# Optimization experiments

Hardware: AMD Instinct MI355X
Metric: run time of the kernel (lower is better)

## Reference

```python
import jax, jax.numpy as jnp
import numpy as np

N, H, O, E, K = 131072, 128, 128, 8, 2


def setup_inputs() -> dict:
    key = jax.random.key(0)
    k1, k2, k3, k4 = jax.random.split(key, 4)
    x = jax.random.normal(k1, (N, H), dtype=jnp.float32)
    w_gate = jax.random.normal(k2, (H, E), dtype=jnp.float32) * 0.02
    w_noise = jax.random.normal(k3, (H, E), dtype=jnp.float32) * 0.02
    w_expert = jax.random.normal(k4, (E, H, O), dtype=jnp.float32) * (1.0 / np.sqrt(H))
    b_expert = jnp.zeros((E, O), dtype=jnp.float32)
    return {"x": x, "w_gate": w_gate, "w_noise": w_noise,
            "w_expert": w_expert, "b_expert": b_expert, "top_k": K}


def _gates(x, w_gate, top_k):
    # Noisy top-k gating (eval mode: noise term w_noise is inactive).
    logits = x @ w_gate                              # [N, E]
    top_vals, top_idx = jax.lax.top_k(logits, top_k)  # [N, K]
    top_gates = jax.nn.softmax(top_vals, axis=-1)     # renormalize over top-k
    n = logits.shape[0]
    rows = jnp.arange(n)[:, None]                     # [N, 1]
    gates = jnp.zeros_like(logits).at[rows, top_idx].set(top_gates)  # [N, E] sparse
    return gates


def reference(x, w_gate, w_noise, w_expert, b_expert, top_k):
    gates = _gates(x, w_gate, top_k)                                  # [N, E]
    # Dense (mathematically identical) dispatch/combine: every expert FFN
    # applied per token, weighted by its (mostly-zero) gate.
    expert_out = jnp.einsum('nh,eho->neo', x, w_expert) + b_expert     # [N, E, O]
    out = jnp.einsum('ne,neo->no', gates, expert_out)                  # [N, O]
    return out
```

## Files before the change

kernel.cpp:

```cpp
#include <hip/hip_runtime.h>
#include <math.h>

typedef __bf16 bf16x8 __attribute__((ext_vector_type(8)));
typedef float f32x16 __attribute__((ext_vector_type(16)));

#define NTOK 131072
#define HDIM 128
#define ODIM 128
#define NEXP 8

__device__ __forceinline__ unsigned short f2bf(float f){
  union { float f; unsigned u; } v; v.f = f;
  unsigned r = v.u + 0x7FFFu + ((v.u >> 16) & 1u);
  return (unsigned short)(r >> 16);
}

__global__ void pack_w(const float* __restrict__ we, const float* __restrict__ be,
                       unsigned short* __restrict__ pw){
  int f = blockIdx.x * 256 + threadIdx.x;
  int l  = f & 63;
  int kt = (f >> 6) % 9;
  int emt = f / (64 * 9);
  int mt = emt & 3;
  int e  = emt >> 2;
  int o  = (mt << 5) + (l & 31);
  unsigned short vals[8];
#pragma unroll
  for (int j = 0; j < 8; ++j){
    int kl = ((l >> 5) << 3) + j;
    float v;
    if (kt < 8){
      int h = kt * 16 + kl;
      v = we[(e * HDIM + h) * ODIM + o];
    } else {
      v = (kl == 0) ? be[e * ODIM + o] : 0.0f;
    }
    vals[j] = f2bf(v);
  }
  *(bf16x8*)(pw + (size_t)f * 8) = *(bf16x8*)vals;
}

__launch_bounds__(256, 2)
__global__ void moe_fused(const float* __restrict__ x, const float* __restrict__ wg,
                          const unsigned short* __restrict__ pw, float* __restrict__ out){
  __shared__ char lds[33792 + 4096 + 2048];
  float* xs            = (float*)lds;
  unsigned short* frag = (unsigned short*)lds;
  float* tb            = (float*)lds;
  float* wgl           = (float*)(lds + 33792);
  float* glds          = (float*)(lds + 33792 + 4096);

  int t = threadIdx.x;
  size_t tokbase = (size_t)blockIdx.x * 64;

  ((float4*)wgl)[t] = ((const float4*)wg)[t];
  {
    const float4* xsrc = (const float4*)(x + tokbase * HDIM);
#pragma unroll
    for (int i = 0; i < 8; ++i){
      int idx = i * 256 + t;
      int tok = idx >> 5, c = idx & 31;
      *(float4*)&xs[tok * 132 + c * 4] = xsrc[idx];
    }
  }
  __syncthreads();

  float4 cv[8];
#pragma unroll
  for (int i = 0; i < 8; ++i)
    cv[i] = *(float4*)&xs[(t >> 2) * 132 + (t & 3) * 32 + i * 4];

  if (t < 64){
    float lg[8];
#pragma unroll
    for (int e = 0; e < 8; ++e) lg[e] = 0.0f;
#pragma unroll 8
    for (int c = 0; c < 32; ++c){
      float4 v = *(float4*)&xs[t * 132 + c * 4];
      const float* wr = wgl + c * 32;
#pragma unroll
      for (int e = 0; e < 8; ++e)
        lg[e] += v.x * wr[e] + v.y * wr[8 + e] + v.z * wr[16 + e] + v.w * wr[24 + e];
    }
    int i1 = 0; float v1 = lg[0];
#pragma unroll
    for (int e = 1; e < 8; ++e) if (lg[e] > v1){ v1 = lg[e]; i1 = e; }
    int i2 = -1; float v2 = -3.4e38f;
#pragma unroll
    for (int e = 0; e < 8; ++e) if (e != i1 && lg[e] > v2){ v2 = lg[e]; i2 = e; }
    float ex = __expf(v2 - v1);
    float inv = 1.0f / (1.0f + ex);
#pragma unroll
    for (int e = 0; e < 8; ++e)
      glds[e * 64 + t] = (e == i1) ? inv : ((e == i2) ? ex * inv : 0.0f);
  }
  __syncthreads();

  {
    int tokL = t >> 2, q = t & 3, tg = tokL >> 5;
#pragma unroll
    for (int jb = 0; jb < 4; ++jb){
      int h0 = q * 32 + jb * 8;
      int kt = h0 >> 4;
      int lslot = (tokL & 31) + 32 * ((h0 >> 3) & 1);
      float4 a = cv[2 * jb], b = cv[2 * jb + 1];
      unsigned long long lo = (unsigned long long)f2bf(a.x)
                            | ((unsigned long long)f2bf(a.y) << 16)
                            | ((unsigned long long)f2bf(a.z) << 32)
                            | ((unsigned long long)f2bf(a.w) << 48);
      unsigned long long hi = (unsigned long long)f2bf(b.x)
                            | ((unsigned long long)f2bf(b.y) << 16)
                            | ((unsigned long long)f2bf(b.z) << 32)
                            | ((unsigned long long)f2bf(b.w) << 48);
      unsigned long long* dst =
        (unsigned long long*)&frag[(((tg * 9) + kt) * 64 + lslot) * 8];
      dst[0] = lo; dst[1] = hi;
    }
    if (t < 128){
      int btg = t >> 6, bl = t & 63;
      unsigned long long* dst =
        (unsigned long long*)&frag[(((btg * 9) + 8) * 64 + bl) * 8];
      dst[0] = (bl < 32) ? 0x3F80ull : 0ull;
      dst[1] = 0ull;
    }
  }
  __syncthreads();

  int w = t >> 6, l = t & 63, l32 = l & 31, lh = l >> 5;

  bf16x8 xb0[9], xb1[9];
#pragma unroll
  for (int kt = 0; kt < 9; ++kt){
    xb0[kt] = *(const bf16x8*)&frag[((0 * 9 + kt) * 64 + l) * 8];
    xb1[kt] = *(const bf16x8*)&frag[((1 * 9 + kt) * 64 + l) * 8];
  }
  __syncthreads();

  f32x16 zero16;
#pragma unroll
  for (int i = 0; i < 16; ++i) zero16[i] = 0.0f;
  f32x16 tot0 = zero16, tot1 = zero16;

  const bf16x8* pwp = (const bf16x8*)pw;
#pragma unroll 1
  for (int e = 0; e < 8; ++e){
    float g0 = glds[e * 64 + l32];
    float g1 = glds[e * 64 + 32 + l32];
    const bf16x8* ap = pwp + ((size_t)(e * 4 + w) * 9) * 64 + l;
    f32x16 p0 = zero16, p1 = zero16;
#pragma unroll
    for (int kt = 0; kt < 9; ++kt){
      bf16x8 a = ap[kt * 64];
      p0 = __builtin_amdgcn_mfma_f32_32x32x16_bf16(a, xb0[kt], p0, 0, 0, 0);
      p1 = __builtin_amdgcn_mfma_f32_32x32x16_bf16(a, xb1[kt], p1, 0, 0, 0);
    }
#pragma unroll
    for (int r = 0; r < 16; ++r){
      tot0[r] += g0 * p0[r];
      tot1[r] += g1 * p1[r];
    }
  }

  {
#pragma unroll
    for (int rg = 0; rg < 4; ++rg){
      int o = w * 32 + rg * 8 + lh * 4;
      {
        int trow = 0 * 32 + l32;
        int cs = (o >> 2) ^ l32;
        *(float4*)&tb[trow * 128 + cs * 4] =
          make_float4(tot0[rg * 4 + 0], tot0[rg * 4 + 1], tot0[rg * 4 + 2], tot0[rg * 4 + 3]);
      }
      {
        int trow = 1 * 32 + l32;
        int cs = (o >> 2) ^ l32;
        *(float4*)&tb[trow * 128 + cs * 4] =
          make_float4(tot1[rg * 4 + 0], tot1[rg * 4 + 1], tot1[rg * 4 + 2], tot1[rg * 4 + 3]);
      }
    }
  }
  __syncthreads();
#pragma unroll
  for (int i = 0; i < 8; ++i){
    int idx = i * 256 + t;
    int trow = idx >> 5, c = idx & 31;
    int cs = c ^ (trow & 31);
    float4 v = *(float4*)&tb[trow * 128 + cs * 4];
    *(float4*)(out + (tokbase + trow) * ODIM + c * 4) = v;
  }
}

extern "C" void kernel_launch(void* const* d_in, const int* in_sizes, int n_in,
                              void* d_out, int out_size, void* d_ws, size_t ws_size,
                              hipStream_t stream){
  const float* x  = (const float*)d_in[0];
  const float* wg = (const float*)d_in[1];
  const float* we = (const float*)d_in[3];
  const float* be = (const float*)d_in[4];
  float* out = (float*)d_out;

  unsigned short* pw = (unsigned short*)d_ws;

  pack_w   <<<72,   256, 0, stream>>>(we, be, pw);
  moe_fused<<<2048, 256, 0, stream>>>(x, wg, pw, out);
}
```

Before: 161.3 us.

## Split MoE into gating/pack and LDS-staged weight GEMM kernels

Splits the fused kernel in two. One kernel computes the gates with a 4-way parallel logit reduction and writes bf16 MFMA-fragment x and transposed gates to workspace. A second GEMM kernel stages half of one output tile's expert weights in LDS and processes 512 tokens per block, reusing those weights across 16 token groups instead of reloading them from global memory per 64 tokens. The bias moves out of the MFMA k-loop into a scalar epilogue. The cost is an extra kernel launch plus a global round trip for the bf16 x fragments and the gates.

```diff
diff --git a/kernel.cpp b/kernel.cpp
--- a/kernel.cpp
+++ b/kernel.cpp
@@ -15,41 +15,27 @@
   return (unsigned short)(r >> 16);
 }
 
-__global__ void pack_w(const float* __restrict__ we, const float* __restrict__ be,
-                       unsigned short* __restrict__ pw){
+__global__ void pack_w(const float* __restrict__ we, unsigned short* __restrict__ pw){
   int f = blockIdx.x * 256 + threadIdx.x;
-  int l  = f & 63;
-  int kt = (f >> 6) % 9;
-  int emt = f / (64 * 9);
-  int mt = emt & 3;
-  int e  = emt >> 2;
-  int o  = (mt << 5) + (l & 31);
+  int l   = f & 63;
+  int kt2 = (f >> 6) & 3;
+  int e   = (f >> 8) & 7;
+  int h   = (f >> 11) & 1;
+  int ot  = (f >> 12) & 3;
+  int o = ot * 32 + (l & 31);
+  int kbase = (h * 4 + kt2) * 16 + ((l >> 5) << 3);
   unsigned short vals[8];
 #pragma unroll
-  for (int j = 0; j < 8; ++j){
-    int kl = ((l >> 5) << 3) + j;
-    float v;
-    if (kt < 8){
-      int h = kt * 16 + kl;
-      v = we[(e * HDIM + h) * ODIM + o];
-    } else {
-      v = (kl == 0) ? be[e * ODIM + o] : 0.0f;
-    }
-    vals[j] = f2bf(v);
-  }
+  for (int j = 0; j < 8; ++j)
+    vals[j] = f2bf(we[(e * HDIM + kbase + j) * ODIM + o]);
   *(bf16x8*)(pw + (size_t)f * 8) = *(bf16x8*)vals;
 }
 
-__launch_bounds__(256, 2)
-__global__ void moe_fused(const float* __restrict__ x, const float* __restrict__ wg,
-                          const unsigned short* __restrict__ pw, float* __restrict__ out){
-  __shared__ char lds[33792 + 4096 + 2048];
-  float* xs            = (float*)lds;
-  unsigned short* frag = (unsigned short*)lds;
-  float* tb            = (float*)lds;
-  float* wgl           = (float*)(lds + 33792);
-  float* glds          = (float*)(lds + 33792 + 4096);
-
+__global__ void gating_pack(const float* __restrict__ x, const float* __restrict__ wg,
+                            float* __restrict__ gates_t, unsigned short* __restrict__ xf){
+  __shared__ float xs[64 * 128];
+  __shared__ float wgl[128 * 8];
+  __shared__ float plg[64 * 36];
   int t = threadIdx.x;
   size_t tokbase = (size_t)blockIdx.x * 64;
 
@@ -60,28 +46,35 @@
     for (int i = 0; i < 8; ++i){
       int idx = i * 256 + t;
       int tok = idx >> 5, c = idx & 31;
-      *(float4*)&xs[tok * 132 + c * 4] = xsrc[idx];
+      *(float4*)&xs[tok * 128 + ((c ^ (tok & 7)) << 2)] = xsrc[idx];
     }
   }
   __syncthreads();
 
-  float4 cv[8];
-#pragma unroll
-  for (int i = 0; i < 8; ++i)
-    cv[i] = *(float4*)&xs[(t >> 2) * 132 + (t & 3) * 32 + i * 4];
+  {
+    int tok = t & 63, q = t >> 6;
+    float lg[8];
+#pragma unroll
+    for (int e = 0; e < 8; ++e) lg[e] = 0.0f;
+#pragma unroll
+    for (int i = 0; i < 8; ++i){
+      int c = q * 8 + i;
+      float4 v = *(float4*)&xs[tok * 128 + ((c ^ (tok & 7)) << 2)];
+      const float* wr = wgl + c * 32;
+#pragma unroll
+      for (int e = 0; e < 8; ++e)
+        lg[e] += v.x * wr[e] + v.y * wr[8 + e] + v.z * wr[16 + e] + v.w * wr[24 + e];
+    }
+    *(float4*)&plg[tok * 36 + q * 8]     = make_float4(lg[0], lg[1], lg[2], lg[3]);
+    *(float4*)&plg[tok * 36 + q * 8 + 4] = make_float4(lg[4], lg[5], lg[6], lg[7]);
+  }
+  __syncthreads();
 
   if (t < 64){
     float lg[8];
 #pragma unroll
-    for (int e = 0; e < 8; ++e) lg[e] = 0.0f;
-#pragma unroll 8
-    for (int c = 0; c < 32; ++c){
-      float4 v = *(float4*)&xs[t * 132 + c * 4];
-      const float* wr = wgl + c * 32;
-#pragma unroll
-      for (int e = 0; e < 8; ++e)
-        lg[e] += v.x * wr[e] + v.y * wr[8 + e] + v.z * wr[16 + e] + v.w * wr[24 + e];
-    }
+    for (int e = 0; e < 8; ++e)
+      lg[e] = plg[t * 36 + e] + plg[t * 36 + 8 + e] + plg[t * 36 + 16 + e] + plg[t * 36 + 24 + e];
     int i1 = 0; float v1 = lg[0];
 #pragma unroll
     for (int e = 1; e < 8; ++e) if (lg[e] > v1){ v1 = lg[e]; i1 = e; }
@@ -92,17 +85,21 @@
     float inv = 1.0f / (1.0f + ex);
 #pragma unroll
     for (int e = 0; e < 8; ++e)
-      glds[e * 64 + t] = (e == i1) ? inv : ((e == i2) ? ex * inv : 0.0f);
-  }
-  __syncthreads();
+      gates_t[(size_t)e * NTOK + tokbase + t] = (e == i1) ? inv : ((e == i2) ? ex * inv : 0.0f);
+  }
 
   {
-    int tokL = t >> 2, q = t & 3, tg = tokL >> 5;
+    int tokL = t >> 2, q = t & 3;
+    float4 cv[8];
+#pragma unroll
+    for (int i = 0; i < 8; ++i)
+      cv[i] = *(float4*)&xs[tokL * 128 + (((q * 8 + i) ^ (tokL & 7)) << 2)];
+    size_t tgG = (size_t)blockIdx.x * 2 + (tokL >> 5);
 #pragma unroll
     for (int jb = 0; jb < 4; ++jb){
       int h0 = q * 32 + jb * 8;
       int kt = h0 >> 4;
-      int lslot = (tokL & 31) + 32 * ((h0 >> 3) & 1);
+      int lslot = (tokL & 31) + 32 * (jb & 1);
       float4 a = cv[2 * jb], b = cv[2 * jb + 1];
       unsigned long long lo = (unsigned long long)f2bf(a.x)
                             | ((unsigned long long)f2bf(a.y) << 16)
@@ -112,82 +109,120 @@
                             | ((unsigned long long)f2bf(b.y) << 16)
                             | ((unsigned long long)f2bf(b.z) << 32)
                             | ((unsigned long long)f2bf(b.w) << 48);
-      unsigned long long* dst =
-        (unsigned long long*)&frag[(((tg * 9) + kt) * 64 + lslot) * 8];
+      unsigned long long* dst = (unsigned long long*)(xf + ((tgG * 8 + kt) * 64 + lslot) * 8);
       dst[0] = lo; dst[1] = hi;
     }
-    if (t < 128){
-      int btg = t >> 6, bl = t & 63;
-      unsigned long long* dst =
-        (unsigned long long*)&frag[(((btg * 9) + 8) * 64 + bl) * 8];
-      dst[0] = (bl < 32) ? 0x3F80ull : 0ull;
-      dst[1] = 0ull;
-    }
-  }
-  __syncthreads();
-
+  }
+}
+
+__launch_bounds__(256, 2)
+__global__ void moe_gemm(const unsigned short* __restrict__ pw,
+                         const unsigned short* __restrict__ xf,
+                         const float* __restrict__ gates_t,
+                         const float* __restrict__ be, float* __restrict__ out){
+  __shared__ unsigned short Wh[16384];
+  __shared__ float glds[8 * 512];
+  __shared__ float blds[256];
+
+  int t = threadIdx.x;
+  int ot = blockIdx.x & 3;
+  int tb = blockIdx.x >> 2;
   int w = t >> 6, l = t & 63, l32 = l & 31, lh = l >> 5;
-
-  bf16x8 xb0[9], xb1[9];
-#pragma unroll
-  for (int kt = 0; kt < 9; ++kt){
-    xb0[kt] = *(const bf16x8*)&frag[((0 * 9 + kt) * 64 + l) * 8];
-    xb1[kt] = *(const bf16x8*)&frag[((1 * 9 + kt) * 64 + l) * 8];
-  }
-  __syncthreads();
+  size_t tokb = (size_t)tb * 512;
+
+#pragma unroll
+  for (int it = 0; it < 4; ++it){
+    int idx = it * 256 + t;
+    int e = idx >> 7, c = idx & 127;
+    *(float4*)&glds[e * 512 + c * 4] =
+      *(const float4*)&gates_t[(size_t)e * NTOK + tokb + c * 4];
+  }
+  blds[t] = be[(t >> 5) * ODIM + ot * 32 + (t & 31)];
 
   f32x16 zero16;
 #pragma unroll
   for (int i = 0; i < 16; ++i) zero16[i] = 0.0f;
-  f32x16 tot0 = zero16, tot1 = zero16;
-
-  const bf16x8* pwp = (const bf16x8*)pw;
+  f32x16 tot0 = zero16, tot1 = zero16, tot2 = zero16, tot3 = zero16;
+
 #pragma unroll 1
-  for (int e = 0; e < 8; ++e){
-    float g0 = glds[e * 64 + l32];
-    float g1 = glds[e * 64 + 32 + l32];
-    const bf16x8* ap = pwp + ((size_t)(e * 4 + w) * 9) * 64 + l;
-    f32x16 p0 = zero16, p1 = zero16;
-#pragma unroll
-    for (int kt = 0; kt < 9; ++kt){
-      bf16x8 a = ap[kt * 64];
-      p0 = __builtin_amdgcn_mfma_f32_32x32x16_bf16(a, xb0[kt], p0, 0, 0, 0);
-      p1 = __builtin_amdgcn_mfma_f32_32x32x16_bf16(a, xb1[kt], p1, 0, 0, 0);
-    }
-#pragma unroll
-    for (int r = 0; r < 16; ++r){
-      tot0[r] += g0 * p0[r];
-      tot1[r] += g1 * p1[r];
-    }
-  }
-
-  {
-#pragma unroll
-    for (int rg = 0; rg < 4; ++rg){
-      int o = w * 32 + rg * 8 + lh * 4;
+  for (int h = 0; h < 2; ++h){
+    {
+      const uint4* wsrc = (const uint4*)(pw + (size_t)(ot * 2 + h) * 16384);
+      uint4* wdst = (uint4*)Wh;
+#pragma unroll
+      for (int it = 0; it < 8; ++it)
+        wdst[it * 256 + t] = wsrc[it * 256 + t];
+    }
+    bf16x8 xb[4][4];
+#pragma unroll
+    for (int tg = 0; tg < 4; ++tg){
+      size_t tgG = tokb / 32 + w * 4 + tg;
+#pragma unroll
+      for (int kt = 0; kt < 4; ++kt)
+        xb[tg][kt] = *(const bf16x8*)(xf + ((tgG * 8 + h * 4 + kt) * 64 + l) * 8);
+    }
+    __syncthreads();
+
+#pragma unroll 1
+    for (int e = 0; e < 8; ++e){
+      float g0 = glds[e * 512 + (w * 4 + 0) * 32 + l32];
+      float g1 = glds[e * 512 + (w * 4 + 1) * 32 + l32];
+      float g2 = glds[e * 512 + (w * 4 + 2) * 32 + l32];
+      float g3 = glds[e * 512 + (w * 4 + 3) * 32 + l32];
       {
-        int trow = 0 * 32 + l32;
-        int cs = (o >> 2) ^ l32;
-        *(float4*)&tb[trow * 128 + cs * 4] =
-          make_float4(tot0[rg * 4 + 0], tot0[rg * 4 + 1], tot0[rg * 4 + 2], tot0[rg * 4 + 3]);
+        f32x16 p0 = zero16, p1 = zero16;
+#pragma unroll
+        for (int kt = 0; kt < 4; ++kt){
+          bf16x8 a = *(const bf16x8*)&Wh[((e * 4 + kt) * 64 + l) * 8];
+          p0 = __builtin_amdgcn_mfma_f32_32x32x16_bf16(a, xb[0][kt], p0, 0, 0, 0);
+          p1 = __builtin_amdgcn_mfma_f32_32x32x16_bf16(a, xb[1][kt], p1, 0, 0, 0);
+        }
+#pragma unroll
+        for (int r = 0; r < 16; ++r){ tot0[r] += g0 * p0[r]; tot1[r] += g1 * p1[r]; }
       }
       {
-        int trow = 1 * 32 + l32;
-        int cs = (o >> 2) ^ l32;
-        *(float4*)&tb[trow * 128 + cs * 4] =
-          make_float4(tot1[rg * 4 + 0], tot1[rg * 4 + 1], tot1[rg * 4 + 2], tot1[rg * 4 + 3]);
+        f32x16 p0 = zero16, p1 = zero16;
+#pragma unroll
+        for (int kt = 0; kt < 4; ++kt){
+          bf16x8 a = *(const bf16x8*)&Wh[((e * 4 + kt) * 64 + l) * 8];
+          p0 = __builtin_amdgcn_mfma_f32_32x32x16_bf16(a, xb[2][kt], p0, 0, 0, 0);
+          p1 = __builtin_amdgcn_mfma_f32_32x32x16_bf16(a, xb[3][kt], p1, 0, 0, 0);
+        }
+#pragma unroll
+        for (int r = 0; r < 16; ++r){ tot2[r] += g2 * p0[r]; tot3[r] += g3 * p1[r]; }
       }
     }
-  }
-  __syncthreads();
-#pragma unroll
-  for (int i = 0; i < 8; ++i){
-    int idx = i * 256 + t;
-    int trow = idx >> 5, c = idx & 31;
-    int cs = c ^ (trow & 31);
-    float4 v = *(float4*)&tb[trow * 128 + cs * 4];
-    *(float4*)(out + (tokbase + trow) * ODIM + c * 4) = v;
-  }
+    __syncthreads();
+  }
+
+#pragma unroll
+  for (int e = 0; e < 8; ++e){
+    float bb[16];
+#pragma unroll
+    for (int rg = 0; rg < 4; ++rg){
+      float4 b4 = *(float4*)&blds[e * 32 + rg * 8 + lh * 4];
+      bb[rg * 4 + 0] = b4.x; bb[rg * 4 + 1] = b4.y; bb[rg * 4 + 2] = b4.z; bb[rg * 4 + 3] = b4.w;
+    }
+    float g0 = glds[e * 512 + (w * 4 + 0) * 32 + l32];
+    float g1 = glds[e * 512 + (w * 4 + 1) * 32 + l32];
+    float g2 = glds[e * 512 + (w * 4 + 2) * 32 + l32];
+    float g3 = glds[e * 512 + (w * 4 + 3) * 32 + l32];
+#pragma unroll
+    for (int r = 0; r < 16; ++r){
+      tot0[r] += g0 * bb[r]; tot1[r] += g1 * bb[r];
+      tot2[r] += g2 * bb[r]; tot3[r] += g3 * bb[r];
+    }
+  }
+#define STORE_TG(tg, tot)                                                       \
+  {                                                                             \
+    float* orow = out + (tokb + (size_t)(w * 4 + tg) * 32 + l32) * ODIM + ot * 32; \
+    _Pragma("unroll")                                                           \
+    for (int rg = 0; rg < 4; ++rg)                                              \
+      *(float4*)(orow + rg * 8 + lh * 4) =                                      \
+        make_float4(tot[rg * 4 + 0], tot[rg * 4 + 1], tot[rg * 4 + 2], tot[rg * 4 + 3]); \
+  }
+  STORE_TG(0, tot0) STORE_TG(1, tot1) STORE_TG(2, tot2) STORE_TG(3, tot3)
+#undef STORE_TG
 }
 
 extern "C" void kernel_launch(void* const* d_in, const int* in_sizes, int n_in,
@@ -199,8 +234,11 @@
   const float* be = (const float*)d_in[4];
   float* out = (float*)d_out;
 
-  unsigned short* pw = (unsigned short*)d_ws;
-
-  pack_w   <<<72,   256, 0, stream>>>(we, be, pw);
-  moe_fused<<<2048, 256, 0, stream>>>(x, wg, pw, out);
-}
+  unsigned short* pw      = (unsigned short*)d_ws;
+  float*          gates_t = (float*)((char*)d_ws + 262144);
+  unsigned short* xf      = (unsigned short*)((char*)d_ws + 4456448);
+
+  pack_w     <<<64,   256, 0, stream>>>(we, pw);
+  gating_pack<<<2048, 256, 0, stream>>>(x, wg, gates_t, xf);
+  moe_gemm   <<<1024, 256, 0, stream>>>(pw, xf, gates_t, be, out);
+}
```

New measurement: 165.7 us. 1.03x slower.
